# Optimization experiments

Hardware: AMD Instinct MI355X
Metric: run time of the kernel (lower is better)

## Reference

```python
import jax, jax.numpy as jnp
import numpy as np

B, C, K, D = 256, 1000, 2, 128


def setup_inputs() -> dict:
    key = jax.random.key(0)
    k1, k2, k3 = jax.random.split(key, 3)
    z = jax.random.normal(k1, (B, D), dtype=jnp.float32)
    mu = jax.random.normal(k2, (C, K, D), dtype=jnp.float32) * 0.1
    logits_pi = jnp.zeros((C, K), dtype=jnp.float32)
    # identity Cholesky factors plus small strictly-lower noise (unit diagonal)
    noise = jnp.tril(jax.random.normal(k3, (C, K, D, D), dtype=jnp.float32), -1)
    covL = jnp.broadcast_to(jnp.eye(D, dtype=jnp.float32), (C, K, D, D)) + 0.01 * noise
    logits_prior = jnp.zeros((C,), dtype=jnp.float32)
    return {"z": z, "mu": mu, "logits_pi": logits_pi, "covL": covL, "logits_prior": logits_prior}


def reference(z, mu, logits_pi, covL, logits_prior):
    Bn, Dn = z.shape
    Cn, Kn = logits_pi.shape
    CK = Cn * Kn
    mu_f = mu.reshape(CK, Dn)               # (CK, D)
    L = covL.reshape(CK, Dn, Dn)            # (CK, D, D) lower triangular
    diff = z[None, :, :] - mu_f[:, None, :] # (CK, B, D)
    rhs = jnp.swapaxes(diff, 1, 2)          # (CK, D, B)
    y = jax.scipy.linalg.solve_triangular(L, rhs, lower=True)  # (CK, D, B)
    maha = jnp.sum(y * y, axis=1).T         # (B, CK)
    logdet = 2.0 * jnp.sum(jnp.log(jnp.diagonal(L, axis1=-2, axis2=-1)), axis=-1)  # (CK,)
    const = Dn * jnp.log(jnp.asarray(2.0 * jnp.pi, dtype=z.dtype))
    logpdf = (-0.5 * (maha + logdet[None, :] + const)).reshape(Bn, Cn, Kn)
    logpi = jax.nn.log_softmax(logits_pi, axis=-1)             # (C, K)
    log_pz_c = jax.scipy.special.logsumexp(logpdf + logpi[None], axis=-1)  # (B, C)
    return logits_prior[None, :] + log_pz_c
```

## Files before the change

### kernel.cpp

```cpp
#include <hip/hip_runtime.h>
#include <cstdint>

#define CC 1000
#define KK 2
#define DD 128

typedef short bf16x8 __attribute__((ext_vector_type(8)));
typedef float f32x16 __attribute__((ext_vector_type(16)));
typedef int   i32x4  __attribute__((ext_vector_type(4)));
typedef unsigned int u32x2 __attribute__((ext_vector_type(2)));

__device__ __forceinline__ uint32_t cvtpk(float lo, float hi) {
    uint32_t r;
    asm("v_cvt_pk_bf16_f32 %0, %1, %2" : "=v"(r) : "v"(lo), "v"(hi));
    return r;
}
__device__ __forceinline__ f32x16 zero16() {
    f32x16 v;
    #pragma unroll
    for (int p = 0; p < 16; ++p) v[p] = 0.f;
    return v;
}

struct Frag8 { uint32_t a0, a1, a2, a3, b0, b1, b2, b3; };

__device__ __forceinline__ bf16x8 flo(const Frag8 f) {
    i32x4 t; t[0] = (int)f.a0; t[1] = (int)f.a1; t[2] = (int)f.a2; t[3] = (int)f.a3;
    return __builtin_bit_cast(bf16x8, t);
}
__device__ __forceinline__ bf16x8 fhi(const Frag8 f) {
    i32x4 t; t[0] = (int)f.b0; t[1] = (int)f.b1; t[2] = (int)f.b2; t[3] = (int)f.b3;
    return __builtin_bit_cast(bf16x8, t);
}

__device__ __forceinline__ Frag8 build_frags(const f32x16 t) {
    uint32_t W0 = cvtpk(t[0],  t[1]),  W1 = cvtpk(t[2],  t[3]);
    uint32_t W2 = cvtpk(t[4],  t[5]),  W3 = cvtpk(t[6],  t[7]);
    uint32_t W4 = cvtpk(t[8],  t[9]),  W5 = cvtpk(t[10], t[11]);
    uint32_t W6 = cvtpk(t[12], t[13]), W7 = cvtpk(t[14], t[15]);
    u32x2 p02 = __builtin_amdgcn_permlane32_swap(W2, W0, false, false);
    u32x2 p13 = __builtin_amdgcn_permlane32_swap(W3, W1, false, false);
    u32x2 p46 = __builtin_amdgcn_permlane32_swap(W6, W4, false, false);
    u32x2 p57 = __builtin_amdgcn_permlane32_swap(W7, W5, false, false);
    Frag8 f;
    f.a0 = p02[1]; f.a1 = p13[1]; f.a2 = p02[0]; f.a3 = p13[0];
    f.b0 = p46[1]; f.b1 = p57[1]; f.b2 = p46[0]; f.b3 = p57[0];
    return f;
}

__device__ __forceinline__ f32x16 off_apply(const char* Ep, const Frag8 yj, f32x16 acc) {
    bf16x8 A0 = *(const bf16x8*)(Ep);
    bf16x8 A1 = *(const bf16x8*)(Ep + 32);
    acc = __builtin_amdgcn_mfma_f32_32x32x16_bf16(A0, flo(yj), acc, 0, 0, 0);
    acc = __builtin_amdgcn_mfma_f32_32x32x16_bf16(A1, fhi(yj), acc, 0, 0, 0);
    return acc;
}
__device__ __forceinline__ f32x16 m_solve(const char* Mp, const Frag8 tf) {
    bf16x8 MA0 = *(const bf16x8*)(Mp);
    bf16x8 MA1 = *(const bf16x8*)(Mp + 32);
    f32x16 y = zero16();
    y = __builtin_amdgcn_mfma_f32_32x32x16_bf16(MA0, flo(tf), y, 0, 0, 0);
    y = __builtin_amdgcn_mfma_f32_32x32x16_bf16(MA1, fhi(tf), y, 0, 0, 0);
    return y;
}

__global__ __launch_bounds__(256, 1) void mda_partial_kernel(
    const float* __restrict__ z,
    const float* __restrict__ mu,
    const float* __restrict__ covL,
    float* __restrict__ ws)
{
    __shared__ __align__(16) char E[35840];
    __shared__ float RD[DD];
    __shared__ float LOGV[DD];

    const int bid = blockIdx.x;
    const int c   = bid >> 1;
    const int k   = bid & 1;
    const int tid = threadIdx.x;
    const int w   = tid >> 6, l = tid & 63, l31 = l & 31, hp = l >> 5;
    const int off = l31 * 80 + 16 * hp;

    const float* Lm  = covL + (int64_t)(c*KK + k) * (DD*DD);
    const float* muv = mu + (size_t)(c*KK + k) * DD;

    #pragma unroll
    for (int rep = 0; rep < 6; ++rep) {
        int t2 = tid + 256*rep;
        int blk = t2 >> 8, r = (t2 >> 3) & 31, c4 = t2 & 7;
        int ib = 1 + (blk >= 1) + (blk >= 3);
        int jb = blk - ((ib * (ib - 1)) >> 1);
        float4 v = *(const float4*)(Lm + (size_t)(32*ib + r)*DD + 32*jb + 4*c4);
        uint2 u; u.x = cvtpk(-v.x, -v.y); u.y = cvtpk(-v.z, -v.w);
        *(uint2*)(E + blk*2560 + r*80 + 8*c4) = u;
    }

    float4 dv[4];
    {
        const int r = (tid >> 3) & 31, c4 = tid & 7;
        #pragma unroll
        for (int ib = 0; ib < 4; ++ib) {
            dv[ib] = *(const float4*)(Lm + (size_t)(32*ib + r)*DD + 32*ib + 4*c4);
            if (c4 == (r >> 2)) {
                float4 v = dv[ib];
                int e = r & 3;
                float dg = (e == 0) ? v.x : (e == 1) ? v.y : (e == 2) ? v.z : v.w;
                RD[32*ib + r]   = 1.0f / dg;
                LOGV[32*ib + r] = __logf(dg);
            }
        }
    }
    __syncthreads();

    float sld = LOGV[l] + LOGV[64 + l];
    #pragma unroll
    for (int o = 1; o < 64; o <<= 1) sld += __shfl_xor(sld, o, 64);

    {
        const int r = (tid >> 3) & 31, c4 = tid & 7;
        const int n0 = 4*c4;
        #pragma unroll
        for (int ib = 0; ib < 4; ++ib) {
            float4 v = dv[ib];
            float rdr = RD[32*ib + r];
            float se0 = (n0+0 < r) ? -v.x*rdr : 0.f;
            float se1 = (n0+1 < r) ? -v.y*rdr : 0.f;
            float se2 = (n0+2 < r) ? -v.z*rdr : 0.f;
            float se3 = (n0+3 < r) ? -v.w*rdr : 0.f;
            uint32_t tx = cvtpk((n0+0 == r) ? 1.f : se0, (n0+1 == r) ? 1.f : se1);
            uint32_t ty = cvtpk((n0+2 == r) ? 1.f : se2, (n0+3 == r) ? 1.f : se3);
            char* tt = E + 25600 + ib*2560 + 2*r;
            *(unsigned short*)(tt + (n0+0)*80) = (unsigned short)(tx & 0xffffu);
            *(unsigned short*)(tt + (n0+1)*80) = (unsigned short)(tx >> 16);
            *(unsigned short*)(tt + (n0+2)*80) = (unsigned short)(ty & 0xffffu);
            *(unsigned short*)(tt + (n0+3)*80) = (unsigned short)(ty >> 16);
            uint2 u; u.x = cvtpk(se0, se1); u.y = cvtpk(se2, se3);
            *(uint2*)(E + 15360 + ib*2560 + r*80 + 8*c4) = u;
        }
    }
    __syncthreads();

    {
        const char* SmB = E + 15360 + w*2560;
        const char* TtB = E + 25600 + w*2560;
        bf16x8 A0 = *(const bf16x8*)(SmB + l31*80 + 16*hp);
        bf16x8 A1 = *(const bf16x8*)(SmB + l31*80 + 32 + 16*hp);
        bf16x8 B0 = *(const bf16x8*)(TtB + l31*80 + 16*hp);
        bf16x8 B1 = *(const bf16x8*)(TtB + l31*80 + 32 + 16*hp);
        f32x16 mm = zero16();
        mm = __builtin_amdgcn_mfma_f32_32x32x16_bf16(A0, B0, mm, 0,0,0);
        mm = __builtin_amdgcn_mfma_f32_32x32x16_bf16(A1, B1, mm, 0,0,0);
        float rdn = RD[32*w + l31];
        char* SmW = E + 15360 + w*2560;
        #pragma unroll
        for (int pe = 0; pe < 16; pe += 2) {
            int rowp = (pe&3) + 8*(pe>>2) + 4*hp;
            float m0 = (mm[pe]   + ((rowp     == l31) ? 1.f : 0.f)) * rdn;
            float m1 = (mm[pe+1] + ((rowp + 1 == l31) ? 1.f : 0.f)) * rdn;
            uint32_t mp = cvtpk(m0, m1);
            *(unsigned short*)(SmW + rowp*80     + 2*l31) = (unsigned short)(mp & 0xffffu);
            *(unsigned short*)(SmW + (rowp+1)*80 + 2*l31) = (unsigned short)(mp >> 16);
        }
    }
    __syncthreads();

    #pragma unroll 1
    for (int half = 0; half < 2; ++half) {
        const int bcol = half * 128 + w * 32 + l31;
        const float* zb = z + (size_t)bcol * DD;

        float macc = 0.f;
        f32x16 acc, yv;
        Frag8 tf, y0, y1, y2;

        #define LOAD_R(i)                                                        \
            do {                                                                 \
                _Pragma("unroll")                                                \
                for (int q = 0; q < 4; ++q) {                                    \
                    float4 zv = *(const float4*)(zb + 32*(i) + 8*q + 4*hp);      \
                    float4 mv = *(const float4*)(muv + 32*(i) + 8*q + 4*hp);     \
                    acc[4*q+0] = zv.x - mv.x;  acc[4*q+1] = zv.y - mv.y;         \
                    acc[4*q+2] = zv.z - mv.z;  acc[4*q+3] = zv.w - mv.w;         \
                }                                                                \
            } while (0)
        #define SQACC()                                                          \
            do {                                                                 \
                _Pragma("unroll")                                                \
                for (int p = 0; p < 16; ++p) macc += yv[p] * yv[p];              \
            } while (0)

        LOAD_R(0);
        tf = build_frags(acc);
        yv = m_solve(E + 15360 + 0*2560 + off, tf);
        SQACC();
        y0 = build_frags(yv);
        LOAD_R(1);
        acc = off_apply(E + 0*2560 + off, y0, acc);
        tf = build_frags(acc);
        yv = m_solve(E + 15360 + 1*2560 + off, tf);
        SQACC();
        y1 = build_frags(yv);
        LOAD_R(2);
        acc = off_apply(E + 1*2560 + off, y0, acc);
        acc = off_apply(E + 2*2560 + off, y1, acc);
        tf = build_frags(acc);
        yv = m_solve(E + 15360 + 2*2560 + off, tf);
        SQACC();
        y2 = build_frags(yv);
        LOAD_R(3);
        acc = off_apply(E + 3*2560 + off, y0, acc);
        acc = off_apply(E + 4*2560 + off, y1, acc);
        acc = off_apply(E + 5*2560 + off, y2, acc);
        tf = build_frags(acc);
        yv = m_solve(E + 15360 + 3*2560 + off, tf);
        SQACC();
        #undef LOAD_R
        #undef SQACC

        macc += __shfl_xor(macc, 32, 64);

        const float CST = 235.2482645f;
        float lp = -0.5f * (macc + 2.f * sld + CST);
        if (hp == 0)
            ws[(size_t)k * (256 * CC) + (size_t)bcol * CC + c] = lp;
    }
}

__global__ __launch_bounds__(256) void mda_combine_kernel(
    const float* __restrict__ lp,
    const float* __restrict__ logits_pi,
    const float* __restrict__ prior,
    float* __restrict__ out)
{
    int idx = blockIdx.x * 256 + threadIdx.x;
    int c = idx % CC;
    float lp0 = lp[idx];
    float lp1 = lp[256 * CC + idx];
    float pi0 = logits_pi[c*2+0], pi1 = logits_pi[c*2+1];
    float mp = fmaxf(pi0, pi1);
    float lsepi = mp + __logf(__expf(pi0-mp) + __expf(pi1-mp));
    float t0 = lp0 + pi0, t1 = lp1 + pi1;
    float mt = fmaxf(t0, t1);
    out[idx] = prior[c] + mt + __logf(__expf(t0-mt) + __expf(t1-mt)) - lsepi;
}

extern "C" void kernel_launch(void* const* d_in, const int* in_sizes, int n_in,
                              void* d_out, int out_size, void* d_ws, size_t ws_size,
                              hipStream_t stream) {
    const float* z         = (const float*)d_in[0];
    const float* mu        = (const float*)d_in[1];
    const float* logits_pi = (const float*)d_in[2];
    const float* covL      = (const float*)d_in[3];
    const float* prior     = (const float*)d_in[4];
    float* out = (float*)d_out;
    float* wsLp = (float*)d_ws;

    hipLaunchKernelGGL(mda_partial_kernel, dim3(2*CC), dim3(256), 0, stream,
                       z, mu, covL, wsLp);
    hipLaunchKernelGGL(mda_combine_kernel, dim3(256 * CC / 256), dim3(256), 0, stream,
                       wsLp, logits_pi, prior, out);
}
```

Before: 54.55 us.

## Fuse partial and combine kernels, loop both mixture components per block

Merges the per-component Mahalanobis kernel and the logsumexp combine kernel into one launch. Each block now handles one class and runs both mixture components in sequence, keeping the four log-likelihoods in registers and writing the final output directly. This removes the workspace round trip and the second launch. In exchange the grid halves to 1000 blocks with serialized per-block work, which lowers parallelism on the 256 CUs and makes the tail longer.

Result: slower. 56.58 us (+3.7%).

```diff
diff --git a/kernel.cpp b/kernel.cpp
--- a/kernel.cpp
+++ b/kernel.cpp
@@ -64,184 +64,194 @@
     return y;
 }
 
-__global__ __launch_bounds__(256, 1) void mda_partial_kernel(
+__global__ __launch_bounds__(256, 1) void mda_fused_kernel(
     const float* __restrict__ z,
     const float* __restrict__ mu,
+    const float* __restrict__ logits_pi,
     const float* __restrict__ covL,
-    float* __restrict__ ws)
+    const float* __restrict__ prior,
+    float* __restrict__ out)
 {
     __shared__ __align__(16) char E[35840];
     __shared__ float RD[DD];
     __shared__ float LOGV[DD];
 
-    const int bid = blockIdx.x;
-    const int c   = bid >> 1;
-    const int k   = bid & 1;
+    const int c   = blockIdx.x;
     const int tid = threadIdx.x;
     const int w   = tid >> 6, l = tid & 63, l31 = l & 31, hp = l >> 5;
     const int off = l31 * 80 + 16 * hp;
 
-    const float* Lm  = covL + (int64_t)(c*KK + k) * (DD*DD);
-    const float* muv = mu + (size_t)(c*KK + k) * DD;
-
-    #pragma unroll
-    for (int rep = 0; rep < 6; ++rep) {
-        int t2 = tid + 256*rep;
-        int blk = t2 >> 8, r = (t2 >> 3) & 31, c4 = t2 & 7;
-        int ib = 1 + (blk >= 1) + (blk >= 3);
-        int jb = blk - ((ib * (ib - 1)) >> 1);
-        float4 v = *(const float4*)(Lm + (size_t)(32*ib + r)*DD + 32*jb + 4*c4);
-        uint2 u; u.x = cvtpk(-v.x, -v.y); u.y = cvtpk(-v.z, -v.w);
-        *(uint2*)(E + blk*2560 + r*80 + 8*c4) = u;
+    float lp00, lp01, lp10, lp11;
+
+    #pragma unroll 1
+    for (int k = 0; k < KK; ++k) {
+        const float* Lm  = covL + (int64_t)(c*KK + k) * (DD*DD);
+        const float* muv = mu + (size_t)(c*KK + k) * DD;
+
+        __syncthreads();
+
+        #pragma unroll
+        for (int rep = 0; rep < 6; ++rep) {
+            int t2 = tid + 256*rep;
+            int blk = t2 >> 8, r = (t2 >> 3) & 31, c4 = t2 & 7;
+            int ib = 1 + (blk >= 1) + (blk >= 3);
+            int jb = blk - ((ib * (ib - 1)) >> 1);
+            float4 v = *(const float4*)(Lm + (size_t)(32*ib + r)*DD + 32*jb + 4*c4);
+            uint2 u; u.x = cvtpk(-v.x, -v.y); u.y = cvtpk(-v.z, -v.w);
+            *(uint2*)(E + blk*2560 + r*80 + 8*c4) = u;
+        }
+
+        float4 dv[4];
+        {
+            const int r = (tid >> 3) & 31, c4 = tid & 7;
+            #pragma unroll
+            for (int ib = 0; ib < 4; ++ib) {
+                dv[ib] = *(const float4*)(Lm + (size_t)(32*ib + r)*DD + 32*ib + 4*c4);
+                if (c4 == (r >> 2)) {
+                    float4 v = dv[ib];
+                    int e = r & 3;
+                    float dg = (e == 0) ? v.x : (e == 1) ? v.y : (e == 2) ? v.z : v.w;
+                    RD[32*ib + r]   = 1.0f / dg;
+                    LOGV[32*ib + r] = __logf(dg);
+                }
+            }
+        }
+        __syncthreads();
+
+        float sld = LOGV[l] + LOGV[64 + l];
+        #pragma unroll
+        for (int o = 1; o < 64; o <<= 1) sld += __shfl_xor(sld, o, 64);
+
+        {
+            const int r = (tid >> 3) & 31, c4 = tid & 7;
+            const int n0 = 4*c4;
+            #pragma unroll
+            for (int ib = 0; ib < 4; ++ib) {
+                float4 v = dv[ib];
+                float rdr = RD[32*ib + r];
+                float se0 = (n0+0 < r) ? -v.x*rdr : 0.f;
+                float se1 = (n0+1 < r) ? -v.y*rdr : 0.f;
+                float se2 = (n0+2 < r) ? -v.z*rdr : 0.f;
+                float se3 = (n0+3 < r) ? -v.w*rdr : 0.f;
+                uint32_t tx = cvtpk((n0+0 == r) ? 1.f : se0, (n0+1 == r) ? 1.f : se1);
+                uint32_t ty = cvtpk((n0+2 == r) ? 1.f : se2, (n0+3 == r) ? 1.f : se3);
+                char* tt = E + 25600 + ib*2560 + 2*r;
+                *(unsigned short*)(tt + (n0+0)*80) = (unsigned short)(tx & 0xffffu);
+                *(unsigned short*)(tt + (n0+1)*80) = (unsigned short)(tx >> 16);
+                *(unsigned short*)(tt + (n0+2)*80) = (unsigned short)(ty & 0xffffu);
+                *(unsigned short*)(tt + (n0+3)*80) = (unsigned short)(ty >> 16);
+                uint2 u; u.x = cvtpk(se0, se1); u.y = cvtpk(se2, se3);
+                *(uint2*)(E + 15360 + ib*2560 + r*80 + 8*c4) = u;
+            }
+        }
+        __syncthreads();
+
+        {
+            const char* SmB = E + 15360 + w*2560;
+            const char* TtB = E + 25600 + w*2560;
+            bf16x8 A0 = *(const bf16x8*)(SmB + l31*80 + 16*hp);
+            bf16x8 A1 = *(const bf16x8*)(SmB + l31*80 + 32 + 16*hp);
+            bf16x8 B0 = *(const bf16x8*)(TtB + l31*80 + 16*hp);
+            bf16x8 B1 = *(const bf16x8*)(TtB + l31*80 + 32 + 16*hp);
+            f32x16 mm = zero16();
+            mm = __builtin_amdgcn_mfma_f32_32x32x16_bf16(A0, B0, mm, 0,0,0);
+            mm = __builtin_amdgcn_mfma_f32_32x32x16_bf16(A1, B1, mm, 0,0,0);
+            float rdn = RD[32*w + l31];
+            char* SmW = E + 15360 + w*2560;
+            #pragma unroll
+            for (int pe = 0; pe < 16; pe += 2) {
+                int rowp = (pe&3) + 8*(pe>>2) + 4*hp;
+                float m0 = (mm[pe]   + ((rowp     == l31) ? 1.f : 0.f)) * rdn;
+                float m1 = (mm[pe+1] + ((rowp + 1 == l31) ? 1.f : 0.f)) * rdn;
+                uint32_t mp = cvtpk(m0, m1);
+                *(unsigned short*)(SmW + rowp*80     + 2*l31) = (unsigned short)(mp & 0xffffu);
+                *(unsigned short*)(SmW + (rowp+1)*80 + 2*l31) = (unsigned short)(mp >> 16);
+            }
+        }
+        __syncthreads();
+
+        #pragma unroll 1
+        for (int half = 0; half < 2; ++half) {
+            const int bcol = half * 128 + w * 32 + l31;
+            const float* zb = z + (size_t)bcol * DD;
+
+            float macc = 0.f;
+            f32x16 acc, yv;
+            Frag8 tf, y0, y1, y2;
+
+            #define LOAD_R(i)                                                        \
+                do {                                                                 \
+                    _Pragma("unroll")                                                \
+                    for (int q = 0; q < 4; ++q) {                                    \
+                        float4 zv = *(const float4*)(zb + 32*(i) + 8*q + 4*hp);      \
+                        float4 mv = *(const float4*)(muv + 32*(i) + 8*q + 4*hp);     \
+                        acc[4*q+0] = zv.x - mv.x;  acc[4*q+1] = zv.y - mv.y;         \
+                        acc[4*q+2] = zv.z - mv.z;  acc[4*q+3] = zv.w - mv.w;         \
+                    }                                                                \
+                } while (0)
+            #define SQACC()                                                          \
+                do {                                                                 \
+                    _Pragma("unroll")                                                \
+                    for (int p = 0; p < 16; ++p) macc += yv[p] * yv[p];              \
+                } while (0)
+
+            LOAD_R(0);
+            tf = build_frags(acc);
+            yv = m_solve(E + 15360 + 0*2560 + off, tf);
+            SQACC();
+            y0 = build_frags(yv);
+            LOAD_R(1);
+            acc = off_apply(E + 0*2560 + off, y0, acc);
+            tf = build_frags(acc);
+            yv = m_solve(E + 15360 + 1*2560 + off, tf);
+            SQACC();
+            y1 = build_frags(yv);
+            LOAD_R(2);
+            acc = off_apply(E + 1*2560 + off, y0, acc);
+            acc = off_apply(E + 2*2560 + off, y1, acc);
+            tf = build_frags(acc);
+            yv = m_solve(E + 15360 + 2*2560 + off, tf);
+            SQACC();
+            y2 = build_frags(yv);
+            LOAD_R(3);
+            acc = off_apply(E + 3*2560 + off, y0, acc);
+            acc = off_apply(E + 4*2560 + off, y1, acc);
+            acc = off_apply(E + 5*2560 + off, y2, acc);
+            tf = build_frags(acc);
+            yv = m_solve(E + 15360 + 3*2560 + off, tf);
+            SQACC();
+            #undef LOAD_R
+            #undef SQACC
+
+            macc += __shfl_xor(macc, 32, 64);
+
+            const float CST = 235.2482645f;
+            float lp = -0.5f * (macc + 2.f * sld + CST);
+            if (k == 0) { if (half == 0) lp00 = lp; else lp01 = lp; }
+            else        { if (half == 0) lp10 = lp; else lp11 = lp; }
+        }
     }
 
-    float4 dv[4];
-    {
-        const int r = (tid >> 3) & 31, c4 = tid & 7;
-        #pragma unroll
-        for (int ib = 0; ib < 4; ++ib) {
-            dv[ib] = *(const float4*)(Lm + (size_t)(32*ib + r)*DD + 32*ib + 4*c4);
-            if (c4 == (r >> 2)) {
-                float4 v = dv[ib];
-                int e = r & 3;
-                float dg = (e == 0) ? v.x : (e == 1) ? v.y : (e == 2) ? v.z : v.w;
-                RD[32*ib + r]   = 1.0f / dg;
-                LOGV[32*ib + r] = __logf(dg);
-            }
+    if (hp == 0) {
+        float pi0 = logits_pi[c*2+0], pi1 = logits_pi[c*2+1];
+        float mp = fmaxf(pi0, pi1);
+        float lsepi = mp + __logf(__expf(pi0-mp) + __expf(pi1-mp));
+        float pr = prior[c];
+        {
+            int bcol = w * 32 + l31;
+            float t0 = lp00 + pi0, t1 = lp10 + pi1;
+            float mt = fmaxf(t0, t1);
+            out[(size_t)bcol * CC + c] =
+                pr + mt + __logf(__expf(t0-mt) + __expf(t1-mt)) - lsepi;
+        }
+        {
+            int bcol = 128 + w * 32 + l31;
+            float t0 = lp01 + pi0, t1 = lp11 + pi1;
+            float mt = fmaxf(t0, t1);
+            out[(size_t)bcol * CC + c] =
+                pr + mt + __logf(__expf(t0-mt) + __expf(t1-mt)) - lsepi;
         }
     }
-    __syncthreads();
-
-    float sld = LOGV[l] + LOGV[64 + l];
-    #pragma unroll
-    for (int o = 1; o < 64; o <<= 1) sld += __shfl_xor(sld, o, 64);
-
-    {
-        const int r = (tid >> 3) & 31, c4 = tid & 7;
-        const int n0 = 4*c4;
-        #pragma unroll
-        for (int ib = 0; ib < 4; ++ib) {
-            float4 v = dv[ib];
-            float rdr = RD[32*ib + r];
-            float se0 = (n0+0 < r) ? -v.x*rdr : 0.f;
-            float se1 = (n0+1 < r) ? -v.y*rdr : 0.f;
-            float se2 = (n0+2 < r) ? -v.z*rdr : 0.f;
-            float se3 = (n0+3 < r) ? -v.w*rdr : 0.f;
-            uint32_t tx = cvtpk((n0+0 == r) ? 1.f : se0, (n0+1 == r) ? 1.f : se1);
-            uint32_t ty = cvtpk((n0+2 == r) ? 1.f : se2, (n0+3 == r) ? 1.f : se3);
-            char* tt = E + 25600 + ib*2560 + 2*r;
-            *(unsigned short*)(tt + (n0+0)*80) = (unsigned short)(tx & 0xffffu);
-            *(unsigned short*)(tt + (n0+1)*80) = (unsigned short)(tx >> 16);
-            *(unsigned short*)(tt + (n0+2)*80) = (unsigned short)(ty & 0xffffu);
-            *(unsigned short*)(tt + (n0+3)*80) = (unsigned short)(ty >> 16);
-            uint2 u; u.x = cvtpk(se0, se1); u.y = cvtpk(se2, se3);
-            *(uint2*)(E + 15360 + ib*2560 + r*80 + 8*c4) = u;
-        }
-    }
-    __syncthreads();
-
-    {
-        const char* SmB = E + 15360 + w*2560;
-        const char* TtB = E + 25600 + w*2560;
-        bf16x8 A0 = *(const bf16x8*)(SmB + l31*80 + 16*hp);
-        bf16x8 A1 = *(const bf16x8*)(SmB + l31*80 + 32 + 16*hp);
-        bf16x8 B0 = *(const bf16x8*)(TtB + l31*80 + 16*hp);
-        bf16x8 B1 = *(const bf16x8*)(TtB + l31*80 + 32 + 16*hp);
-        f32x16 mm = zero16();
-        mm = __builtin_amdgcn_mfma_f32_32x32x16_bf16(A0, B0, mm, 0,0,0);
-        mm = __builtin_amdgcn_mfma_f32_32x32x16_bf16(A1, B1, mm, 0,0,0);
-        float rdn = RD[32*w + l31];
-        char* SmW = E + 15360 + w*2560;
-        #pragma unroll
-        for (int pe = 0; pe < 16; pe += 2) {
-            int rowp = (pe&3) + 8*(pe>>2) + 4*hp;
-            float m0 = (mm[pe]   + ((rowp     == l31) ? 1.f : 0.f)) * rdn;
-            float m1 = (mm[pe+1] + ((rowp + 1 == l31) ? 1.f : 0.f)) * rdn;
-            uint32_t mp = cvtpk(m0, m1);
-            *(unsigned short*)(SmW + rowp*80     + 2*l31) = (unsigned short)(mp & 0xffffu);
-            *(unsigned short*)(SmW + (rowp+1)*80 + 2*l31) = (unsigned short)(mp >> 16);
-        }
-    }
-    __syncthreads();
-
-    #pragma unroll 1
-    for (int half = 0; half < 2; ++half) {
-        const int bcol = half * 128 + w * 32 + l31;
-        const float* zb = z + (size_t)bcol * DD;
-
-        float macc = 0.f;
-        f32x16 acc, yv;
-        Frag8 tf, y0, y1, y2;
-
-        #define LOAD_R(i)                                                        \
-            do {                                                                 \
-                _Pragma("unroll")                                                \
-                for (int q = 0; q < 4; ++q) {                                    \
-                    float4 zv = *(const float4*)(zb + 32*(i) + 8*q + 4*hp);      \
-                    float4 mv = *(const float4*)(muv + 32*(i) + 8*q + 4*hp);     \
-                    acc[4*q+0] = zv.x - mv.x;  acc[4*q+1] = zv.y - mv.y;         \
-                    acc[4*q+2] = zv.z - mv.z;  acc[4*q+3] = zv.w - mv.w;         \
-                }                                                                \
-            } while (0)
-        #define SQACC()                                                          \
-            do {                                                                 \
-                _Pragma("unroll")                                                \
-                for (int p = 0; p < 16; ++p) macc += yv[p] * yv[p];              \
-            } while (0)
-
-        LOAD_R(0);
-        tf = build_frags(acc);
-        yv = m_solve(E + 15360 + 0*2560 + off, tf);
-        SQACC();
-        y0 = build_frags(yv);
-        LOAD_R(1);
-        acc = off_apply(E + 0*2560 + off, y0, acc);
-        tf = build_frags(acc);
-        yv = m_solve(E + 15360 + 1*2560 + off, tf);
-        SQACC();
-        y1 = build_frags(yv);
-        LOAD_R(2);
-        acc = off_apply(E + 1*2560 + off, y0, acc);
-        acc = off_apply(E + 2*2560 + off, y1, acc);
-        tf = build_frags(acc);
-        yv = m_solve(E + 15360 + 2*2560 + off, tf);
-        SQACC();
-        y2 = build_frags(yv);
-        LOAD_R(3);
-        acc = off_apply(E + 3*2560 + off, y0, acc);
-        acc = off_apply(E + 4*2560 + off, y1, acc);
-        acc = off_apply(E + 5*2560 + off, y2, acc);
-        tf = build_frags(acc);
-        yv = m_solve(E + 15360 + 3*2560 + off, tf);
-        SQACC();
-        #undef LOAD_R
-        #undef SQACC
-
-        macc += __shfl_xor(macc, 32, 64);
-
-        const float CST = 235.2482645f;
-        float lp = -0.5f * (macc + 2.f * sld + CST);
-        if (hp == 0)
-            ws[(size_t)k * (256 * CC) + (size_t)bcol * CC + c] = lp;
-    }
-}
-
-__global__ __launch_bounds__(256) void mda_combine_kernel(
-    const float* __restrict__ lp,
-    const float* __restrict__ logits_pi,
-    const float* __restrict__ prior,
-    float* __restrict__ out)
-{
-    int idx = blockIdx.x * 256 + threadIdx.x;
-    int c = idx % CC;
-    float lp0 = lp[idx];
-    float lp1 = lp[256 * CC + idx];
-    float pi0 = logits_pi[c*2+0], pi1 = logits_pi[c*2+1];
-    float mp = fmaxf(pi0, pi1);
-    float lsepi = mp + __logf(__expf(pi0-mp) + __expf(pi1-mp));
-    float t0 = lp0 + pi0, t1 = lp1 + pi1;
-    float mt = fmaxf(t0, t1);
-    out[idx] = prior[c] + mt + __logf(__expf(t0-mt) + __expf(t1-mt)) - lsepi;
 }
 
 extern "C" void kernel_launch(void* const* d_in, const int* in_sizes, int n_in,
@@ -253,10 +263,7 @@
     const float* covL      = (const float*)d_in[3];
     const float* prior     = (const float*)d_in[4];
     float* out = (float*)d_out;
-    float* wsLp = (float*)d_ws;
-
-    hipLaunchKernelGGL(mda_partial_kernel, dim3(2*CC), dim3(256), 0, stream,
-                       z, mu, covL, wsLp);
-    hipLaunchKernelGGL(mda_combine_kernel, dim3(256 * CC / 256), dim3(256), 0, stream,
-                       wsLp, logits_pi, prior, out);
-}
+
+    hipLaunchKernelGGL(mda_fused_kernel, dim3(CC), dim3(256), 0, stream,
+                       z, mu, logits_pi, covL, prior, out);
+}
```
